# Optimization experiments

Measured on AMD Instinct MI355X. Metric: run time of the kernel, lower is better.

Reference implementation:

```python
import math
import jax, jax.numpy as jnp
import numpy as np

DIM = 512
HEADS = 8
LS = 64  # local_size
SCALE = (DIM // HEADS) ** -0.5


def _normalize(x, eps=1e-12):
    # torch F.normalize(dim=-1): x / max(||x||, eps)
    n = jnp.linalg.norm(x, axis=-1, keepdims=True)
    return x / jnp.maximum(n, eps)


def setup_inputs() -> dict:
    key = jax.random.key(0)
    k0, k1, k2 = jax.random.split(key, 3)
    B, S, D = 8, 4096, DIM
    return {
        "x": jax.random.normal(k0, (B, S, D), jnp.float32),
        "W_qkv": jax.random.normal(k1, (D, 3 * D), jnp.float32) * 0.02,
        "b_qkv": jnp.zeros((3 * D,), jnp.float32),
        "W_proj": jax.random.normal(k2, (D, D), jnp.float32) * 0.02,
        "b_proj": jnp.zeros((D,), jnp.float32),
    }


def reference(x, W_qkv, b_qkv, W_proj, b_proj):
    B, S, D = x.shape
    H = HEADS
    d = D // H
    ls = LS
    nl = S // ls
    ntimes = int(math.log2(nl))

    # qkv projection -> [3, B, H, S, d]
    qkv = (x @ W_qkv + b_qkv).reshape(B, S, 3, H, d).transpose(2, 0, 3, 1, 4)
    q_pre = qkv[0].reshape(B * H, S, d).transpose(0, 2, 1)  # [BH, d, S]

    q_idx_last = jnp.broadcast_to(jnp.arange(S)[None, :], (B * H, S))

    # recursive content-based bipartition (unrolled: ntimes is static)
    for _ in range(ntimes):
        bh, dd, n = q_pre.shape
        q_avg = q_pre.reshape(bh, dd, 2, n // 2).mean(-1)        # [bh, d, 2]
        q_avg = _normalize(q_avg.transpose(0, 2, 1))             # [bh, 2, d]
        q_norm = _normalize(q_pre.transpose(0, 2, 1))            # [bh, n, d]
        # squared euclidean distance [bh, n, 2]
        sq = (jnp.sum(q_norm ** 2, -1)[:, :, None]
              + jnp.sum(q_avg ** 2, -1)[:, None, :]
              - 2.0 * jnp.einsum('bnd,bcd->bnc', q_norm, q_avg))
        q_ratio = (sq[:, :, 0] + 1.0) / (sq[:, :, 1] + 1.0)
        q_idx = jnp.argsort(q_ratio, axis=-1)                    # [bh, n]
        q_idx_last = jnp.take_along_axis(q_idx_last, q_idx, axis=-1).reshape(bh * 2, n // 2)
        q_pre = jnp.take_along_axis(q_pre, q_idx[:, None, :], axis=-1)
        # 'b d (c n) -> (b c) d n' with c=2
        q_pre = q_pre.reshape(bh, dd, 2, n // 2).transpose(0, 2, 1, 3).reshape(bh * 2, dd, n // 2)

    q_idx = q_idx_last.reshape(B, H, S)
    q_idx_rev = jnp.argsort(q_idx, axis=-1)

    # gather qkv along token dim with routed permutation
    qkv_pre = jnp.take_along_axis(qkv, q_idx[None, :, :, :, None], axis=3)  # [3,B,H,S,d]
    # 'qkv b h (nl ls) d -> qkv (b nl) h ls d'
    qkv_pre = qkv_pre.reshape(3, B, H, nl, ls, d).transpose(0, 1, 3, 2, 4, 5).reshape(3, B * nl, H, ls, d)
    q, k, v = qkv_pre[0], qkv_pre[1], qkv_pre[2]

    # windowed diff-softmax-mul attention (softmax over head dim d)
    attn = jax.nn.softmax((q - k) * SCALE, axis=-1)
    out = attn * v                                               # [(B nl), H, ls, d]

    # '(b nl) h ls d -> b h d (nl ls)'
    out = out.reshape(B, nl, H, ls, d).transpose(0, 2, 4, 1, 3).reshape(B, H, d, S)
    out = jnp.take_along_axis(out, q_idx_rev[:, :, None, :], axis=-1)
    res = out.reshape(B, D, S).transpose(0, 2, 1)                # [B, S, D]
    res = res @ W_proj + b_proj
    return x + res
```

## Files before the change

kernel.cpp:

```cpp
#include <hip/hip_runtime.h>
#include <hip/hip_bf16.h>

typedef __bf16 bf16;
typedef __attribute__((ext_vector_type(8))) __bf16 bf16x8;
typedef __attribute__((ext_vector_type(4))) __bf16 bf16x4;
typedef __attribute__((ext_vector_type(4))) float f32x4;

#define M_TOK 32768
#define D_    512
#define N_QKV 1536
#define BK    64
#define SCALE_ 0.125f

#define AS1 __attribute__((address_space(1)))
#define AS3 __attribute__((address_space(3)))

__global__ __launch_bounds__(256) void cvt_bf16(const float* __restrict__ in,
                                                bf16* __restrict__ out, int n4) {
  int i = blockIdx.x * 256 + threadIdx.x;
  if (i >= n4) return;
  f32x4 v = ((const f32x4*)in)[i];
  bf16x4 o;
  o[0] = (bf16)v[0]; o[1] = (bf16)v[1]; o[2] = (bf16)v[2]; o[3] = (bf16)v[3];
  ((bf16x4*)out)[i] = o;
}

template <int PERM>
__global__ __launch_bounds__(256) void transpose_cvt(const float* __restrict__ in,
                                                     bf16* __restrict__ out,
                                                     int K, int N) {
  __shared__ float tile[32][33];
  int n0 = blockIdx.x * 32, k0 = blockIdx.y * 32;
  int tx = threadIdx.x, ty = threadIdx.y;
  for (int i = 0; i < 32; i += 8)
    tile[ty + i][tx] = in[(size_t)(k0 + ty + i) * N + n0 + tx];
  __syncthreads();
  for (int i = 0; i < 32; i += 8) {
    int n = n0 + ty + i;
    int np = n;
    if (PERM) {
      int h = (n & 511) >> 6, qkv = n >> 9;
      np = h * 192 + qkv * 64 + (n & 63);
    }
    out[(size_t)np * K + k0 + tx] = (bf16)tile[tx][ty + i];
  }
}

__global__ __launch_bounds__(256) void gemm_qkv_softmax(const bf16* __restrict__ A,
                                                        const bf16* __restrict__ Bt,
                                                        const float* __restrict__ bqkv,
                                                        bf16* __restrict__ O) {
  __shared__ __align__(16) bf16 sA[128 * BK];
  __shared__ __align__(16) bf16 sB[192 * BK];

  const int tid = threadIdx.x;
  const int w = tid >> 6;
  const int l = tid & 63;
  const int m0 = blockIdx.x * 128;
  const int h  = blockIdx.y;
  const int n0 = h * 192;

  f32x4 acc[2][12];
#pragma unroll
  for (int i = 0; i < 2; ++i)
#pragma unroll
    for (int j = 0; j < 12; ++j) {
      f32x4 z = {0.f, 0.f, 0.f, 0.f};
      acc[i][j] = z;
    }

  const int srow = l >> 3;
  const int schunk = ((l & 7) ^ (l >> 3)) * 8;

  const int fr = l & 15;
  const int fkc = l >> 4;
  const int frs = fr & 7;

  for (int kt = 0; kt < D_; kt += BK) {
#pragma unroll
    for (int q = 0; q < 4; ++q) {
      int rowb = w * 32 + q * 8;
      const bf16* gp = A + (size_t)(m0 + rowb + srow) * D_ + kt + schunk;
      __builtin_amdgcn_global_load_lds((AS1 void*)gp, (AS3 void*)&sA[rowb * BK], 16, 0, 0);
    }
#pragma unroll
    for (int q = 0; q < 6; ++q) {
      int rowb = w * 48 + q * 8;
      const bf16* gp = Bt + (size_t)(n0 + rowb + srow) * D_ + kt + schunk;
      __builtin_amdgcn_global_load_lds((AS1 void*)gp, (AS3 void*)&sB[rowb * BK], 16, 0, 0);
    }
    __syncthreads();

#pragma unroll
    for (int kk = 0; kk < 2; ++kk) {
      const int sw = (((kk << 2) | fkc) ^ frs) * 8;
      bf16x8 af0 = *(const bf16x8*)&sA[(w * 32 + 0  + fr) * BK + sw];
      bf16x8 af1 = *(const bf16x8*)&sA[(w * 32 + 16 + fr) * BK + sw];
#pragma unroll
      for (int j = 0; j < 12; ++j) {
        bf16x8 bfj = *(const bf16x8*)&sB[(j * 16 + fr) * BK + sw];
        acc[0][j] = __builtin_amdgcn_mfma_f32_16x16x32_bf16(af0, bfj, acc[0][j], 0, 0, 0);
        acc[1][j] = __builtin_amdgcn_mfma_f32_16x16x32_bf16(af1, bfj, acc[1][j], 0, 0, 0);
      }
    }
    __syncthreads();
  }

  float bq[4], bk[4], bv[4];
#pragma unroll
  for (int jq = 0; jq < 4; ++jq) {
    int c = h * 64 + jq * 16 + fr;
    bq[jq] = bqkv[c];
    bk[jq] = bqkv[512 + c];
    bv[jq] = bqkv[1024 + c];
  }

  const int rbase = (l >> 4) * 4;
#pragma unroll
  for (int i = 0; i < 2; ++i) {
#pragma unroll
    for (int r = 0; r < 4; ++r) {
      float sc[4];
#pragma unroll
      for (int jq = 0; jq < 4; ++jq)
        sc[jq] = (acc[i][jq][r] + bq[jq] - acc[i][jq + 4][r] - bk[jq]) * SCALE_;
      float mx = fmaxf(fmaxf(sc[0], sc[1]), fmaxf(sc[2], sc[3]));
#pragma unroll
      for (int off = 1; off < 16; off <<= 1) mx = fmaxf(mx, __shfl_xor(mx, off));
      float e[4];
      float sum = 0.f;
#pragma unroll
      for (int jq = 0; jq < 4; ++jq) { e[jq] = __expf(sc[jq] - mx); sum += e[jq]; }
#pragma unroll
      for (int off = 1; off < 16; off <<= 1) sum += __shfl_xor(sum, off);
      float inv = 1.0f / sum;
      int m = m0 + w * 32 + i * 16 + rbase + r;
#pragma unroll
      for (int jq = 0; jq < 4; ++jq) {
        float o = e[jq] * inv * (acc[i][jq + 8][r] + bv[jq]);
        O[(size_t)m * D_ + h * 64 + jq * 16 + fr] = (bf16)o;
      }
    }
  }
}

__global__ __launch_bounds__(256) void gemm_bt_f32(const bf16* __restrict__ A,
                                                   const bf16* __restrict__ Bt,
                                                   const float* __restrict__ bias,
                                                   const float* __restrict__ resid,
                                                   float* __restrict__ C,
                                                   int M, int N, int K) {
  __shared__ __align__(16) bf16 sA[128 * BK];
  __shared__ __align__(16) bf16 sB[128 * BK];

  const int tid = threadIdx.x;
  const int w = tid >> 6;
  const int l = tid & 63;
  const int m0 = blockIdx.x * 128;
  const int n0 = blockIdx.y * 128;
  const int wrow = w >> 1, wcol = w & 1;

  f32x4 acc[4][4];
#pragma unroll
  for (int i = 0; i < 4; ++i)
#pragma unroll
    for (int j = 0; j < 4; ++j) {
      f32x4 z = {0.f, 0.f, 0.f, 0.f};
      acc[i][j] = z;
    }

  const int srow = l >> 3;
  const int schunk = ((l & 7) ^ (l >> 3)) * 8;
  const int fr = l & 15;
  const int fkc = l >> 4;
  const int frs = fr & 7;

  for (int kt = 0; kt < K; kt += BK) {
#pragma unroll
    for (int q = 0; q < 4; ++q) {
      int rowb = w * 32 + q * 8;
      const bf16* gp = A + (size_t)(m0 + rowb + srow) * K + kt + schunk;
      __builtin_amdgcn_global_load_lds((AS1 void*)gp, (AS3 void*)&sA[rowb * BK], 16, 0, 0);
    }
#pragma unroll
    for (int q = 0; q < 4; ++q) {
      int rowb = w * 32 + q * 8;
      const bf16* gp = Bt + (size_t)(n0 + rowb + srow) * K + kt + schunk;
      __builtin_amdgcn_global_load_lds((AS1 void*)gp, (AS3 void*)&sB[rowb * BK], 16, 0, 0);
    }
    __syncthreads();

#pragma unroll
    for (int kk = 0; kk < 2; ++kk) {
      const int sw = (((kk << 2) | fkc) ^ frs) * 8;
      bf16x8 af[4], bfr[4];
#pragma unroll
      for (int i = 0; i < 4; ++i)
        af[i] = *(const bf16x8*)&sA[(wrow * 64 + i * 16 + fr) * BK + sw];
#pragma unroll
      for (int j = 0; j < 4; ++j)
        bfr[j] = *(const bf16x8*)&sB[(wcol * 64 + j * 16 + fr) * BK + sw];
#pragma unroll
      for (int i = 0; i < 4; ++i)
#pragma unroll
        for (int j = 0; j < 4; ++j)
          acc[i][j] = __builtin_amdgcn_mfma_f32_16x16x32_bf16(af[i], bfr[j], acc[i][j], 0, 0, 0);
    }
    __syncthreads();
  }

  const int col = l & 15;
  const int rbase = (l >> 4) * 4;
#pragma unroll
  for (int j = 0; j < 4; ++j) {
    int n = n0 + wcol * 64 + j * 16 + col;
    float bv = bias[n];
#pragma unroll
    for (int i = 0; i < 4; ++i) {
#pragma unroll
      for (int r = 0; r < 4; ++r) {
        int m = m0 + wrow * 64 + i * 16 + rbase + r;
        C[(size_t)m * N + n] = acc[i][j][r] + bv + resid[(size_t)m * N + n];
      }
    }
  }
}

extern "C" void kernel_launch(void* const* d_in, const int* in_sizes, int n_in,
                              void* d_out, int out_size, void* d_ws, size_t ws_size,
                              hipStream_t stream) {
  const float* x     = (const float*)d_in[0];
  const float* Wqkv  = (const float*)d_in[1];
  const float* bqkv  = (const float*)d_in[2];
  const float* Wproj = (const float*)d_in[3];
  const float* bproj = (const float*)d_in[4];
  float* out = (float*)d_out;

  char* ws = (char*)d_ws;
  bf16* Wq_t = (bf16*)ws;
  bf16* Wp_t = (bf16*)(ws + (size_t)N_QKV * D_ * 2);
  char* p = ws + (size_t)N_QKV * D_ * 2 + (size_t)D_ * D_ * 2;
  bf16* Xb = (bf16*)p;
  bf16* O  = (bf16*)(p + (size_t)M_TOK * D_ * 2);

  transpose_cvt<1><<<dim3(N_QKV / 32, D_ / 32), dim3(32, 8), 0, stream>>>(Wqkv, Wq_t, D_, N_QKV);
  transpose_cvt<0><<<dim3(D_ / 32, D_ / 32), dim3(32, 8), 0, stream>>>(Wproj, Wp_t, D_, D_);

  cvt_bf16<<<(M_TOK * D_ / 4 + 255) / 256, 256, 0, stream>>>(x, Xb, M_TOK * D_ / 4);

  gemm_qkv_softmax<<<dim3(M_TOK / 128, 8), 256, 0, stream>>>(Xb, Wq_t, bqkv, O);

  gemm_bt_f32<<<dim3(M_TOK / 128, D_ / 128), 256, 0, stream>>>(
      O, Wp_t, bproj, x, out, M_TOK, D_, D_);
}
```

Measured before the change: 235.2 us.

## Double-buffer LDS tiles with split async prefetch in both GEMMs

Both MFMA GEMM kernels now keep two LDS buffers. The next K-tile is prefetched with global_load_lds while the current tile is consumed: A is staged before the first half of the MFMAs and B between the two halves. Explicit vmcnt waits and raw s_barrier calls replace the two __syncthreads per iteration. MFMA sections are wrapped in s_setprio, and launch bounds request two blocks per CU. The aim is to hide global-load latency behind matrix math, at the cost of doubled LDS use and hand-tuned wait counts that must match the number of loads issued.

After: 226.5 us. -3.7%, faster.

```diff
diff --git a/kernel.cpp b/kernel.cpp
--- a/kernel.cpp
+++ b/kernel.cpp
@@ -46,12 +46,12 @@
   }
 }
 
-__global__ __launch_bounds__(256) void gemm_qkv_softmax(const bf16* __restrict__ A,
-                                                        const bf16* __restrict__ Bt,
-                                                        const float* __restrict__ bqkv,
-                                                        bf16* __restrict__ O) {
-  __shared__ __align__(16) bf16 sA[128 * BK];
-  __shared__ __align__(16) bf16 sB[192 * BK];
+__global__ __launch_bounds__(256, 2) void gemm_qkv_softmax(const bf16* __restrict__ A,
+                                                           const bf16* __restrict__ Bt,
+                                                           const float* __restrict__ bqkv,
+                                                           bf16* __restrict__ O) {
+  __shared__ __align__(16) bf16 sA[2][128 * BK];
+  __shared__ __align__(16) bf16 sB[2][192 * BK];
 
   const int tid = threadIdx.x;
   const int w = tid >> 6;
@@ -76,34 +76,69 @@
   const int fkc = l >> 4;
   const int frs = fr & 7;
 
-  for (int kt = 0; kt < D_; kt += BK) {
-#pragma unroll
-    for (int q = 0; q < 4; ++q) {
-      int rowb = w * 32 + q * 8;
-      const bf16* gp = A + (size_t)(m0 + rowb + srow) * D_ + kt + schunk;
-      __builtin_amdgcn_global_load_lds((AS1 void*)gp, (AS3 void*)&sA[rowb * BK], 16, 0, 0);
-    }
-#pragma unroll
-    for (int q = 0; q < 6; ++q) {
-      int rowb = w * 48 + q * 8;
-      const bf16* gp = Bt + (size_t)(n0 + rowb + srow) * D_ + kt + schunk;
-      __builtin_amdgcn_global_load_lds((AS1 void*)gp, (AS3 void*)&sB[rowb * BK], 16, 0, 0);
-    }
-    __syncthreads();
-
-#pragma unroll
-    for (int kk = 0; kk < 2; ++kk) {
-      const int sw = (((kk << 2) | fkc) ^ frs) * 8;
-      bf16x8 af0 = *(const bf16x8*)&sA[(w * 32 + 0  + fr) * BK + sw];
-      bf16x8 af1 = *(const bf16x8*)&sA[(w * 32 + 16 + fr) * BK + sw];
+  const bf16* gA = A + (size_t)(m0 + w * 32 + srow) * D_ + schunk;
+  const bf16* gB = Bt + (size_t)(n0 + w * 48 + srow) * D_ + schunk;
+
+  auto stageA = [&](int buf, int kt) {
+#pragma unroll
+    for (int q = 0; q < 4; ++q)
+      __builtin_amdgcn_global_load_lds((AS1 const void*)(gA + (size_t)(q * 8) * D_ + kt),
+                                       (AS3 void*)&sA[buf][(w * 32 + q * 8) * BK], 16, 0, 0);
+  };
+  auto stageB = [&](int buf, int kt) {
+#pragma unroll
+    for (int q = 0; q < 6; ++q)
+      __builtin_amdgcn_global_load_lds((AS1 const void*)(gB + (size_t)(q * 8) * D_ + kt),
+                                       (AS3 void*)&sB[buf][(w * 48 + q * 8) * BK], 16, 0, 0);
+  };
+
+  stageA(0, 0);
+  stageB(0, 0);
+
+  const int NT = D_ / BK;
+#pragma unroll
+  for (int t = 0; t < NT; ++t) {
+    const int cur = t & 1;
+    if (t < NT - 1) {
+      stageA(cur ^ 1, (t + 1) * BK);
+      asm volatile("s_waitcnt vmcnt(4)" ::: "memory");
+    } else {
+      asm volatile("s_waitcnt vmcnt(0)" ::: "memory");
+    }
+    __builtin_amdgcn_s_barrier();
+    asm volatile("" ::: "memory");
+
+    {
+      const int sw = (fkc ^ frs) * 8;
+      bf16x8 af0 = *(const bf16x8*)&sA[cur][(w * 32 + 0  + fr) * BK + sw];
+      bf16x8 af1 = *(const bf16x8*)&sA[cur][(w * 32 + 16 + fr) * BK + sw];
+      __builtin_amdgcn_s_setprio(1);
 #pragma unroll
       for (int j = 0; j < 12; ++j) {
-        bf16x8 bfj = *(const bf16x8*)&sB[(j * 16 + fr) * BK + sw];
+        bf16x8 bfj = *(const bf16x8*)&sB[cur][(j * 16 + fr) * BK + sw];
         acc[0][j] = __builtin_amdgcn_mfma_f32_16x16x32_bf16(af0, bfj, acc[0][j], 0, 0, 0);
         acc[1][j] = __builtin_amdgcn_mfma_f32_16x16x32_bf16(af1, bfj, acc[1][j], 0, 0, 0);
       }
-    }
-    __syncthreads();
+      __builtin_amdgcn_s_setprio(0);
+    }
+
+    if (t < NT - 1) stageB(cur ^ 1, (t + 1) * BK);
+
+    {
+      const int sw = ((4 | fkc) ^ frs) * 8;
+      bf16x8 af0 = *(const bf16x8*)&sA[cur][(w * 32 + 0  + fr) * BK + sw];
+      bf16x8 af1 = *(const bf16x8*)&sA[cur][(w * 32 + 16 + fr) * BK + sw];
+      __builtin_amdgcn_s_setprio(1);
+#pragma unroll
+      for (int j = 0; j < 12; ++j) {
+        bf16x8 bfj = *(const bf16x8*)&sB[cur][(j * 16 + fr) * BK + sw];
+        acc[0][j] = __builtin_amdgcn_mfma_f32_16x16x32_bf16(af0, bfj, acc[0][j], 0, 0, 0);
+        acc[1][j] = __builtin_amdgcn_mfma_f32_16x16x32_bf16(af1, bfj, acc[1][j], 0, 0, 0);
+      }
+      __builtin_amdgcn_s_setprio(0);
+    }
+    asm volatile("" ::: "memory");
+    __builtin_amdgcn_s_barrier();
   }
 
   float bq[4], bk[4], bv[4];
@@ -144,14 +179,14 @@
   }
 }
 
-__global__ __launch_bounds__(256) void gemm_bt_f32(const bf16* __restrict__ A,
-                                                   const bf16* __restrict__ Bt,
-                                                   const float* __restrict__ bias,
-                                                   const float* __restrict__ resid,
-                                                   float* __restrict__ C,
-                                                   int M, int N, int K) {
-  __shared__ __align__(16) bf16 sA[128 * BK];
-  __shared__ __align__(16) bf16 sB[128 * BK];
+__global__ __launch_bounds__(256, 2) void gemm_bt_f32(const bf16* __restrict__ A,
+                                                      const bf16* __restrict__ Bt,
+                                                      const float* __restrict__ bias,
+                                                      const float* __restrict__ resid,
+                                                      float* __restrict__ C,
+                                                      int M, int N, int K) {
+  __shared__ __align__(16) bf16 sA[2][128 * BK];
+  __shared__ __align__(16) bf16 sB[2][128 * BK];
 
   const int tid = threadIdx.x;
   const int w = tid >> 6;
@@ -175,38 +210,76 @@
   const int fkc = l >> 4;
   const int frs = fr & 7;
 
-  for (int kt = 0; kt < K; kt += BK) {
-#pragma unroll
-    for (int q = 0; q < 4; ++q) {
-      int rowb = w * 32 + q * 8;
-      const bf16* gp = A + (size_t)(m0 + rowb + srow) * K + kt + schunk;
-      __builtin_amdgcn_global_load_lds((AS1 void*)gp, (AS3 void*)&sA[rowb * BK], 16, 0, 0);
-    }
-#pragma unroll
-    for (int q = 0; q < 4; ++q) {
-      int rowb = w * 32 + q * 8;
-      const bf16* gp = Bt + (size_t)(n0 + rowb + srow) * K + kt + schunk;
-      __builtin_amdgcn_global_load_lds((AS1 void*)gp, (AS3 void*)&sB[rowb * BK], 16, 0, 0);
-    }
-    __syncthreads();
-
-#pragma unroll
-    for (int kk = 0; kk < 2; ++kk) {
-      const int sw = (((kk << 2) | fkc) ^ frs) * 8;
+  const bf16* gA = A + (size_t)(m0 + w * 32 + srow) * K + schunk;
+  const bf16* gB = Bt + (size_t)(n0 + w * 32 + srow) * K + schunk;
+
+  auto stageA = [&](int buf, int kt) {
+#pragma unroll
+    for (int q = 0; q < 4; ++q)
+      __builtin_amdgcn_global_load_lds((AS1 const void*)(gA + (size_t)(q * 8) * K + kt),
+                                       (AS3 void*)&sA[buf][(w * 32 + q * 8) * BK], 16, 0, 0);
+  };
+  auto stageB = [&](int buf, int kt) {
+#pragma unroll
+    for (int q = 0; q < 4; ++q)
+      __builtin_amdgcn_global_load_lds((AS1 const void*)(gB + (size_t)(q * 8) * K + kt),
+                                       (AS3 void*)&sB[buf][(w * 32 + q * 8) * BK], 16, 0, 0);
+  };
+
+  stageA(0, 0);
+  stageB(0, 0);
+
+  const int nt = K / BK;
+  for (int t = 0; t < nt; ++t) {
+    const int cur = t & 1;
+    if (t < nt - 1) {
+      stageA(cur ^ 1, (t + 1) * BK);
+      asm volatile("s_waitcnt vmcnt(4)" ::: "memory");
+    } else {
+      asm volatile("s_waitcnt vmcnt(0)" ::: "memory");
+    }
+    __builtin_amdgcn_s_barrier();
+    asm volatile("" ::: "memory");
+
+    {
+      const int sw = (fkc ^ frs) * 8;
       bf16x8 af[4], bfr[4];
 #pragma unroll
       for (int i = 0; i < 4; ++i)
-        af[i] = *(const bf16x8*)&sA[(wrow * 64 + i * 16 + fr) * BK + sw];
+        af[i] = *(const bf16x8*)&sA[cur][(wrow * 64 + i * 16 + fr) * BK + sw];
 #pragma unroll
       for (int j = 0; j < 4; ++j)
-        bfr[j] = *(const bf16x8*)&sB[(wcol * 64 + j * 16 + fr) * BK + sw];
+        bfr[j] = *(const bf16x8*)&sB[cur][(wcol * 64 + j * 16 + fr) * BK + sw];
+      __builtin_amdgcn_s_setprio(1);
 #pragma unroll
       for (int i = 0; i < 4; ++i)
 #pragma unroll
         for (int j = 0; j < 4; ++j)
           acc[i][j] = __builtin_amdgcn_mfma_f32_16x16x32_bf16(af[i], bfr[j], acc[i][j], 0, 0, 0);
-    }
-    __syncthreads();
+      __builtin_amdgcn_s_setprio(0);
+    }
+
+    if (t < nt - 1) stageB(cur ^ 1, (t + 1) * BK);
+
+    {
+      const int sw = ((4 | fkc) ^ frs) * 8;
+      bf16x8 af[4], bfr[4];
+#pragma unroll
+      for (int i = 0; i < 4; ++i)
+        af[i] = *(const bf16x8*)&sA[cur][(wrow * 64 + i * 16 + fr) * BK + sw];
+#pragma unroll
+      for (int j = 0; j < 4; ++j)
+        bfr[j] = *(const bf16x8*)&sB[cur][(wcol * 64 + j * 16 + fr) * BK + sw];
+      __builtin_amdgcn_s_setprio(1);
+#pragma unroll
+      for (int i = 0; i < 4; ++i)
+#pragma unroll
+        for (int j = 0; j < 4; ++j)
+          acc[i][j] = __builtin_amdgcn_mfma_f32_16x16x32_bf16(af[i], bfr[j], acc[i][j], 0, 0, 0);
+      __builtin_amdgcn_s_setprio(0);
+    }
+    asm volatile("" ::: "memory");
+    __builtin_amdgcn_s_barrier();
   }
 
   const int col = l & 15;
```
